# Kernel tuning notes

Measured on AMD Instinct MI355X. Metric: run time of the kernel, lower is better.

## Reference

```python
import jax, jax.numpy as jnp
import numpy as np

EPS = 1e-6
CONV_P = 3.0
GM_P = 2.0
NUM_NODES = 50000
NUM_EDGES = 600000
NUM_GRAPHS = 512
IN_DIM = 128
HID = 128
OUT_DIM = 64


def _scatter_mean(vals, index, num_segments):
    # scatter_mean with empty segments -> 0 (count clamped to 1)
    s = jax.ops.segment_sum(vals, index, num_segments=num_segments)
    cnt = jax.ops.segment_sum(jnp.ones((vals.shape[0],), vals.dtype), index,
                              num_segments=num_segments)
    return s / jnp.maximum(cnt, 1.0)[:, None]


def _signed_pow(v, p):
    return jnp.sign(v) * (jnp.abs(v) + EPS) ** p


def _spm_conv(x, W, b, src, dst, p):
    h = x @ W.T + b                      # [N, hid] linear
    msg = h[src]                          # gather x_j  [E, hid]
    t = _signed_pow(msg, p)
    pooled = _scatter_mean(t, dst, NUM_NODES)
    return _signed_pow(pooled, 1.0 / p)


def setup_inputs() -> dict:
    key = jax.random.key(0)
    ks = jax.random.split(key, 8)
    x = jax.random.normal(ks[0], (NUM_NODES, IN_DIM), jnp.float32)
    edge_index = jax.random.randint(ks[1], (2, NUM_EDGES), 0, NUM_NODES)
    batch = jnp.sort(jax.random.randint(ks[2], (NUM_NODES,), 0, NUM_GRAPHS))
    s1 = 1.0 / np.sqrt(IN_DIM)
    s2 = 1.0 / np.sqrt(HID)
    W1 = jax.random.uniform(ks[3], (HID, IN_DIM), jnp.float32, -s1, s1)
    b1 = jax.random.uniform(ks[4], (HID,), jnp.float32, -s1, s1)
    W2 = jax.random.uniform(ks[5], (HID, HID), jnp.float32, -s2, s2)
    b2 = jax.random.uniform(ks[6], (HID,), jnp.float32, -s2, s2)
    # final layer: orthogonal-init frozen weight (out_dim=64, hid=128)
    A = jax.random.normal(ks[7], (HID, OUT_DIM), jnp.float32)
    Q, _ = jnp.linalg.qr(A)
    Wout = Q.T                            # [OUT_DIM, HID], orthonormal rows
    bout = jax.random.uniform(jax.random.fold_in(key, 9), (OUT_DIM,),
                              jnp.float32, -s2, s2)
    return {"x": x, "W1": W1, "b1": b1, "W2": W2, "b2": b2,
            "Wout": Wout, "bout": bout, "edge_index": edge_index,
            "batch": batch}


def reference(x, W1, b1, W2, b2, Wout, bout, edge_index, batch):
    src, dst = edge_index[0], edge_index[1]
    h = _spm_conv(x, W1, b1, src, dst, CONV_P)
    h = jax.nn.relu(h)                    # relu between conv layers only
    h = _spm_conv(h, W2, b2, src, dst, CONV_P)
    # global generalized mean pool (signed)
    t = _signed_pow(h, GM_P)
    pooled = _scatter_mean(t, batch, NUM_GRAPHS)
    graph_repr = _signed_pow(pooled, 1.0 / GM_P)   # [G, HID]
    return graph_repr @ Wout.T + bout              # [G, OUT_DIM]
```

## Files before the change

kernel.cpp:

```cpp
#include <hip/hip_runtime.h>
#include <hip/hip_bf16.h>
#include <math.h>

#define N_NODES 50000
#define N_EDGES 600000
#define N_GRAPHS 512
#define DIM 128
#define OUTD 64
#define EPSV 1e-6f
#define BSTRIDE 64
#define EBLK 2344
#define PREP_BLK 64

typedef __attribute__((ext_vector_type(8))) short bf16x8;
typedef __attribute__((ext_vector_type(4))) float f32x4;

__device__ __forceinline__ float sgn(float v) {
    return (v > 0.f) ? 1.f : ((v < 0.f) ? -1.f : 0.f);
}

__device__ __forceinline__ float cube_signed(float v) {
    float m = fabsf(v) + EPSV;
    return sgn(v) * m * m * m;
}

__device__ __forceinline__ float cbrt_pos(float m) {
    return exp2f(log2f(m) * (1.0f / 3.0f));
}

__device__ __forceinline__ unsigned short f2bf(float f) {
    unsigned u = __float_as_uint(f);
    unsigned r = (u + 0x7fff + ((u >> 16) & 1)) >> 16;
    return (unsigned short)r;
}

__device__ __forceinline__ float bf2f(unsigned short h) {
    return __uint_as_float(((unsigned)h) << 16);
}

__device__ __forceinline__ void gather_acc8(const unsigned* __restrict__ T32,
                                            const int* __restrict__ bucket,
                                            int cnt, int lane, float acc[8]) {
    #pragma unroll
    for (int j = 0; j < 8; j++) acc[j] = 0.f;
    if (cnt <= 0) return;
    int myidx = bucket[lane];
    int sub = lane & 15, grp = lane >> 4;
    for (int i = 0; i < cnt; i += 16) {
        uint4 u[4];
        #pragma unroll
        for (int c = 0; c < 4; c++) {
            int eid = i + c * 4 + grp;
            int eidc = eid < cnt - 1 ? eid : cnt - 1;
            int s = __shfl(myidx, eidc, 64);
            u[c] = *(const uint4*)(T32 + (size_t)s * 64 + sub * 4);
        }
        #pragma unroll
        for (int c = 0; c < 4; c++) {
            int eid = i + c * 4 + grp;
            bool ok = eid < cnt;
            unsigned w0 = ok ? u[c].x : 0u;
            unsigned w1 = ok ? u[c].y : 0u;
            unsigned w2 = ok ? u[c].z : 0u;
            unsigned w3 = ok ? u[c].w : 0u;
            acc[0] += __uint_as_float(w0 << 16);
            acc[1] += __uint_as_float(w0 & 0xffff0000u);
            acc[2] += __uint_as_float(w1 << 16);
            acc[3] += __uint_as_float(w1 & 0xffff0000u);
            acc[4] += __uint_as_float(w2 << 16);
            acc[5] += __uint_as_float(w2 & 0xffff0000u);
            acc[6] += __uint_as_float(w3 << 16);
            acc[7] += __uint_as_float(w3 & 0xffff0000u);
        }
    }
    #pragma unroll
    for (int j = 0; j < 8; j++) {
        acc[j] += __shfl_xor(acc[j], 16, 64);
        acc[j] += __shfl_xor(acc[j], 32, 64);
    }
}


__global__ void build(const int* __restrict__ src, const int* __restrict__ dst,
                      int* __restrict__ deg, int* __restrict__ csr,
                      const float* __restrict__ W1, const float* __restrict__ W2,
                      unsigned short* __restrict__ W1hi, unsigned short* __restrict__ W1lo,
                      unsigned short* __restrict__ W2hi, unsigned short* __restrict__ W2lo,
                      const int* __restrict__ batch, int* __restrict__ gstart) {
    int b = blockIdx.x;
    if (b < EBLK) {
        int e = b * 256 + threadIdx.x;
        if (e < N_EDGES) {
            int d = dst[e];
            int slot = atomicAdd(&deg[d], 1);
            if (slot < BSTRIDE) csr[d * BSTRIDE + slot] = src[e];
        }
    } else {
        int i = (b - EBLK) * 256 + threadIdx.x;
        if (i < DIM * DIM) {
            float w = W1[i];
            unsigned short h = f2bf(w);
            W1hi[i] = h;
            W1lo[i] = f2bf(w - bf2f(h));
            w = W2[i];
            h = f2bf(w);
            W2hi[i] = h;
            W2lo[i] = f2bf(w - bf2f(h));
        }
        if (i <= N_GRAPHS) {
            int lo = 0, hi = N_NODES;
            while (lo < hi) {
                int mid = (lo + hi) >> 1;
                if (batch[mid] < i) lo = mid + 1; else hi = mid;
            }
            gstart[i] = lo;
        }
    }
}


__global__ __launch_bounds__(256) void linear_cube_mfma(const float* __restrict__ X,
                                                        const unsigned short* __restrict__ Whi,
                                                        const unsigned short* __restrict__ Wlo,
                                                        const float* __restrict__ B,
                                                        unsigned short* __restrict__ T) {
    int wave = threadIdx.x >> 6;
    int lane = threadIdx.x & 63;
    int tile = blockIdx.x * 4 + wave;
    if (tile >= N_NODES / 16) return;
    int n0 = tile * 16;
    int r = lane & 15;
    int g = lane >> 4;

    bf16x8 xh[4], xl[4];
    const float* xrow = X + (size_t)(n0 + r) * DIM + g * 8;
    #pragma unroll
    for (int kb = 0; kb < 4; kb++) {
        float4 a = *(const float4*)(xrow + kb * 32);
        float4 b = *(const float4*)(xrow + kb * 32 + 4);
        float v[8] = {a.x, a.y, a.z, a.w, b.x, b.y, b.z, b.w};
        #pragma unroll
        for (int j = 0; j < 8; j++) {
            unsigned short h = f2bf(v[j]);
            float rem = v[j] - bf2f(h);
            xh[kb][j] = (short)h;
            xl[kb][j] = (short)f2bf(rem);
        }
    }

    #pragma unroll
    for (int ct = 0; ct < 8; ct++) {
        const unsigned short* whbase = Whi + (size_t)(ct * 16 + r) * DIM + g * 8;
        const unsigned short* wlbase = Wlo + (size_t)(ct * 16 + r) * DIM + g * 8;
        f32x4 acc = {0.f, 0.f, 0.f, 0.f};
        #pragma unroll
        for (int kb = 0; kb < 4; kb++) {
            bf16x8 wh = *(const bf16x8*)(whbase + kb * 32);
            bf16x8 wl = *(const bf16x8*)(wlbase + kb * 32);
            acc = __builtin_amdgcn_mfma_f32_16x16x32_bf16(xh[kb], wh, acc, 0, 0, 0);
            acc = __builtin_amdgcn_mfma_f32_16x16x32_bf16(xl[kb], wh, acc, 0, 0, 0);
            acc = __builtin_amdgcn_mfma_f32_16x16x32_bf16(xh[kb], wl, acc, 0, 0, 0);
        }
        float bias = B[ct * 16 + r];
        #pragma unroll
        for (int q = 0; q < 4; q++) {
            int node = g * 4 + q;
            float h = acc[q] + bias;
            T[(size_t)(n0 + node) * DIM + ct * 16 + r] = f2bf(cube_signed(h));
        }
    }
}


__global__ __launch_bounds__(512) void agg_linear_cube(const unsigned* __restrict__ T32,
                                                       const int* __restrict__ deg,
                                                       const int* __restrict__ csr,
                                                       const unsigned short* __restrict__ Whi,
                                                       const unsigned short* __restrict__ Wlo,
                                                       const float* __restrict__ B,
                                                       unsigned short* __restrict__ Tout) {
    __shared__ float Pl[16][132];
    int wave = threadIdx.x >> 6;
    int lane = threadIdx.x & 63;
    int n0 = blockIdx.x * 16;
    int sub = lane & 15, grp = lane >> 4;

    #pragma unroll
    for (int q = 0; q < 2; q++) {
        int row = wave * 2 + q;
        int nd = n0 + row;
        int d = deg[nd];
        int cnt = d < BSTRIDE ? d : BSTRIDE;
        float acc[8];
        gather_acc8(T32, csr + (size_t)nd * BSTRIDE, cnt, lane, acc);
        float c = (float)(d > 1 ? d : 1);
        float m0 = acc[2 * grp] / c, m1 = acc[2 * grp + 1] / c;
        float r0 = fmaxf(sgn(m0) * cbrt_pos(fabsf(m0) + EPSV), 0.f);
        float r1 = fmaxf(sgn(m1) * cbrt_pos(fabsf(m1) + EPSV), 0.f);
        *(float2*)&Pl[row][sub * 8 + grp * 2] = make_float2(r0, r1);
    }
    __syncthreads();

    int r = lane & 15;
    int g = lane >> 4;
    bf16x8 xh[4], xl[4];
    #pragma unroll
    for (int kb = 0; kb < 4; kb++) {
        float4 va = *(const float4*)&Pl[r][kb * 32 + g * 8];
        float4 vb = *(const float4*)&Pl[r][kb * 32 + g * 8 + 4];
        float v[8] = {va.x, va.y, va.z, va.w, vb.x, vb.y, vb.z, vb.w};
        #pragma unroll
        for (int j = 0; j < 8; j++) {
            unsigned short h = f2bf(v[j]);
            xh[kb][j] = (short)h;
            xl[kb][j] = (short)f2bf(v[j] - bf2f(h));
        }
    }
    int ct = wave;
    const unsigned short* whbase = Whi + (size_t)(ct * 16 + r) * DIM + g * 8;
    const unsigned short* wlbase = Wlo + (size_t)(ct * 16 + r) * DIM + g * 8;
    f32x4 acc = {0.f, 0.f, 0.f, 0.f};
    #pragma unroll
    for (int kb = 0; kb < 4; kb++) {
        bf16x8 wh = *(const bf16x8*)(whbase + kb * 32);
        bf16x8 wl = *(const bf16x8*)(wlbase + kb * 32);
        acc = __builtin_amdgcn_mfma_f32_16x16x32_bf16(xh[kb], wh, acc, 0, 0, 0);
        acc = __builtin_amdgcn_mfma_f32_16x16x32_bf16(xl[kb], wh, acc, 0, 0, 0);
        acc = __builtin_amdgcn_mfma_f32_16x16x32_bf16(xh[kb], wl, acc, 0, 0, 0);
    }
    float bias = B[ct * 16 + r];
    #pragma unroll
    for (int q = 0; q < 4; q++) {
        int node = g * 4 + q;
        float h = acc[q] + bias;
        Tout[(size_t)(n0 + node) * DIM + ct * 16 + r] = f2bf(cube_signed(h));
    }
}


__global__ __launch_bounds__(256) void aggregate(const unsigned* __restrict__ T32,
                                                 const int* __restrict__ deg,
                                                 const int* __restrict__ csr,
                                                 float* __restrict__ P) {
    int nd = blockIdx.x * 4 + (threadIdx.x >> 6);
    if (nd >= N_NODES) return;
    int lane = threadIdx.x & 63;
    int sub = lane & 15, grp = lane >> 4;
    int d = deg[nd];
    int cnt = d < BSTRIDE ? d : BSTRIDE;
    float acc[8];
    gather_acc8(T32, csr + (size_t)nd * BSTRIDE, cnt, lane, acc);
    float c = (float)(d > 1 ? d : 1);
    float m0 = acc[2 * grp] / c, m1 = acc[2 * grp + 1] / c;
    float r0 = sgn(m0) * cbrt_pos(fabsf(m0) + EPSV);
    float r1 = sgn(m1) * cbrt_pos(fabsf(m1) + EPSV);
    *(float2*)(P + (size_t)nd * DIM + sub * 8 + grp * 2) = make_float2(r0, r1);
}


__global__ __launch_bounds__(128) void pool_final(const float* __restrict__ P,
                                                  const int* __restrict__ gstart,
                                                  const float* __restrict__ Wout,
                                                  const float* __restrict__ bout,
                                                  float* __restrict__ out) {
    __shared__ float R[DIM];
    __shared__ float partial[128];
    int g = blockIdx.x, f = threadIdx.x;
    int s = gstart[g], e = gstart[g + 1];
    float acc = 0.f;
    for (int i = s; i < e; i++) {
        float v = P[(size_t)i * DIM + f];
        float m = fabsf(v) + EPSV;
        acc += sgn(v) * m * m;
    }
    int cnt = e - s;
    float c = (float)(cnt > 1 ? cnt : 1);
    float mean = acc / c;
    R[f] = sgn(mean) * sqrtf(fabsf(mean) + EPSV);
    __syncthreads();

    int o = f & 63;
    int half = f >> 6;
    const float4* W4 = (const float4*)Wout + o * 32 + half * 16;
    const float4* R4 = (const float4*)R + half * 16;
    float a = 0.f;
    #pragma unroll
    for (int k = 0; k < 16; k++) {
        float4 w = W4[k];
        float4 r = R4[k];
        a += r.x * w.x + r.y * w.y + r.z * w.z + r.w * w.w;
    }
    partial[f] = a;
    __syncthreads();
    if (f < OUTD) out[(size_t)g * OUTD + f] = bout[f] + partial[f] + partial[f + 64];
}


extern "C" void kernel_launch(void* const* d_in, const int* in_sizes, int n_in,
                              void* d_out, int out_size, void* d_ws, size_t ws_size,
                              hipStream_t stream) {
    const float* x    = (const float*)d_in[0];
    const float* W1   = (const float*)d_in[1];
    const float* b1   = (const float*)d_in[2];
    const float* W2   = (const float*)d_in[3];
    const float* b2   = (const float*)d_in[4];
    const float* Wout = (const float*)d_in[5];
    const float* bout = (const float*)d_in[6];
    const int* edge   = (const int*)d_in[7];
    const int* batch  = (const int*)d_in[8];
    const int* srcp = edge;
    const int* dstp = edge + N_EDGES;
    float* out = (float*)d_out;

    char* ws = (char*)d_ws;
    size_t off = 0;
    auto alloc = [&](size_t bytes) -> char* {
        char* p = ws + off;
        off += (bytes + 255) / 256 * 256;
        return p;
    };
    unsigned short* T1 = (unsigned short*)alloc((size_t)N_NODES * DIM * 2);
    unsigned short* T2 = (unsigned short*)alloc((size_t)N_NODES * DIM * 2);
    float* P        = (float*)alloc((size_t)N_NODES * DIM * 4);
    int*   deg      = (int*)alloc((size_t)N_NODES * 4);
    int*   csr      = (int*)alloc((size_t)N_NODES * BSTRIDE * 4);
    int*   gstart   = (int*)alloc((size_t)(N_GRAPHS + 1) * 4);
    unsigned short* W1hi = (unsigned short*)alloc((size_t)DIM * DIM * 2);
    unsigned short* W1lo = (unsigned short*)alloc((size_t)DIM * DIM * 2);
    unsigned short* W2hi = (unsigned short*)alloc((size_t)DIM * DIM * 2);
    unsigned short* W2lo = (unsigned short*)alloc((size_t)DIM * DIM * 2);

    hipMemsetAsync(deg, 0, (size_t)N_NODES * 4, stream);
    build<<<EBLK + PREP_BLK, 256, 0, stream>>>(srcp, dstp, deg, csr,
                                               W1, W2, W1hi, W1lo, W2hi, W2lo,
                                               batch, gstart);

    const int TILES = N_NODES / 16;
    const int LBLK = (TILES + 3) / 4;
    const int ABLK = (N_NODES + 3) / 4;
    linear_cube_mfma<<<LBLK, 256, 0, stream>>>(x, W1hi, W1lo, b1, T1);
    agg_linear_cube<<<TILES, 512, 0, stream>>>((const unsigned*)T1, deg, csr,
                                               W2hi, W2lo, b2, T2);
    aggregate<<<ABLK, 256, 0, stream>>>((const unsigned*)T2, deg, csr, P);
    pool_final<<<N_GRAPHS, 128, 0, stream>>>(P, gstart, Wout, bout, out);
}
```

Before: 190.6 us.

## Use zero sentinel row to drop per-edge masking in neighbor gather

```diff
diff --git a/kernel.cpp b/kernel.cpp
--- a/kernel.cpp
+++ b/kernel.cpp
@@ -40,43 +40,37 @@
 
 __device__ __forceinline__ void gather_acc8(const unsigned* __restrict__ T32,
                                             const int* __restrict__ bucket,
-                                            int cnt, int lane, float acc[8]) {
-    #pragma unroll
-    for (int j = 0; j < 8; j++) acc[j] = 0.f;
-    if (cnt <= 0) return;
+                                            int cnt16, int lane, float2 acc[4]) {
+    #pragma unroll
+    for (int j = 0; j < 4; j++) acc[j] = make_float2(0.f, 0.f);
+    if (cnt16 <= 0) return;
     int myidx = bucket[lane];
     int sub = lane & 15, grp = lane >> 4;
-    for (int i = 0; i < cnt; i += 16) {
+    for (int i = 0; i < cnt16; i += 16) {
         uint4 u[4];
         #pragma unroll
         for (int c = 0; c < 4; c++) {
-            int eid = i + c * 4 + grp;
-            int eidc = eid < cnt - 1 ? eid : cnt - 1;
-            int s = __shfl(myidx, eidc, 64);
+            int s = __shfl(myidx, i + c * 4 + grp, 64);
             u[c] = *(const uint4*)(T32 + (size_t)s * 64 + sub * 4);
         }
         #pragma unroll
         for (int c = 0; c < 4; c++) {
-            int eid = i + c * 4 + grp;
-            bool ok = eid < cnt;
-            unsigned w0 = ok ? u[c].x : 0u;
-            unsigned w1 = ok ? u[c].y : 0u;
-            unsigned w2 = ok ? u[c].z : 0u;
-            unsigned w3 = ok ? u[c].w : 0u;
-            acc[0] += __uint_as_float(w0 << 16);
-            acc[1] += __uint_as_float(w0 & 0xffff0000u);
-            acc[2] += __uint_as_float(w1 << 16);
-            acc[3] += __uint_as_float(w1 & 0xffff0000u);
-            acc[4] += __uint_as_float(w2 << 16);
-            acc[5] += __uint_as_float(w2 & 0xffff0000u);
-            acc[6] += __uint_as_float(w3 << 16);
-            acc[7] += __uint_as_float(w3 & 0xffff0000u);
-        }
-    }
-    #pragma unroll
-    for (int j = 0; j < 8; j++) {
-        acc[j] += __shfl_xor(acc[j], 16, 64);
-        acc[j] += __shfl_xor(acc[j], 32, 64);
+            acc[0].x += __uint_as_float(u[c].x << 16);
+            acc[0].y += __uint_as_float(u[c].x & 0xffff0000u);
+            acc[1].x += __uint_as_float(u[c].y << 16);
+            acc[1].y += __uint_as_float(u[c].y & 0xffff0000u);
+            acc[2].x += __uint_as_float(u[c].z << 16);
+            acc[2].y += __uint_as_float(u[c].z & 0xffff0000u);
+            acc[3].x += __uint_as_float(u[c].w << 16);
+            acc[3].y += __uint_as_float(u[c].w & 0xffff0000u);
+        }
+    }
+    #pragma unroll
+    for (int j = 0; j < 4; j++) {
+        acc[j].x += __shfl_xor(acc[j].x, 16, 64);
+        acc[j].y += __shfl_xor(acc[j].y, 16, 64);
+        acc[j].x += __shfl_xor(acc[j].x, 32, 64);
+        acc[j].y += __shfl_xor(acc[j].y, 32, 64);
     }
 }
 
@@ -86,17 +80,19 @@
                       const float* __restrict__ W1, const float* __restrict__ W2,
                       unsigned short* __restrict__ W1hi, unsigned short* __restrict__ W1lo,
                       unsigned short* __restrict__ W2hi, unsigned short* __restrict__ W2lo,
-                      const int* __restrict__ batch, int* __restrict__ gstart) {
+                      const int* __restrict__ batch, int* __restrict__ gstart,
+                      unsigned* __restrict__ T1z, unsigned* __restrict__ T2z) {
     int b = blockIdx.x;
     if (b < EBLK) {
         int e = b * 256 + threadIdx.x;
         if (e < N_EDGES) {
             int d = dst[e];
             int slot = atomicAdd(&deg[d], 1);
-            if (slot < BSTRIDE) csr[d * BSTRIDE + slot] = src[e];
+            if (slot < BSTRIDE) csr[d * BSTRIDE + slot] = src[e] + 1;
         }
     } else {
         int i = (b - EBLK) * 256 + threadIdx.x;
+        if (i < 64) { T1z[i] = 0u; T2z[i] = 0u; }
         if (i < DIM * DIM) {
             float w = W1[i];
             unsigned short h = f2bf(w);
@@ -166,7 +162,7 @@
         for (int q = 0; q < 4; q++) {
             int node = g * 4 + q;
             float h = acc[q] + bias;
-            T[(size_t)(n0 + node) * DIM + ct * 16 + r] = f2bf(cube_signed(h));
+            T[(size_t)(n0 + node + 1) * DIM + ct * 16 + r] = f2bf(cube_signed(h));
         }
     }
 }
@@ -179,7 +175,8 @@
                                                        const unsigned short* __restrict__ Wlo,
                                                        const float* __restrict__ B,
                                                        unsigned short* __restrict__ Tout) {
-    __shared__ float Pl[16][132];
+    __shared__ __attribute__((aligned(16))) unsigned Phi[16][68];
+    __shared__ __attribute__((aligned(16))) unsigned Plo[16][68];
     int wave = threadIdx.x >> 6;
     int lane = threadIdx.x & 63;
     int n0 = blockIdx.x * 16;
@@ -191,13 +188,19 @@
         int nd = n0 + row;
         int d = deg[nd];
         int cnt = d < BSTRIDE ? d : BSTRIDE;
-        float acc[8];
-        gather_acc8(T32, csr + (size_t)nd * BSTRIDE, cnt, lane, acc);
+        int cnt16 = (cnt + 15) & ~15;
+        float2 acc[4];
+        gather_acc8(T32, csr + (size_t)nd * BSTRIDE, cnt16, lane, acc);
         float c = (float)(d > 1 ? d : 1);
-        float m0 = acc[2 * grp] / c, m1 = acc[2 * grp + 1] / c;
+        float m0 = acc[grp >> 1].x, m1 = acc[grp >> 1].y;
+        m0 = (grp == 0 ? acc[0].x : grp == 1 ? acc[1].x : grp == 2 ? acc[2].x : acc[3].x) / c;
+        m1 = (grp == 0 ? acc[0].y : grp == 1 ? acc[1].y : grp == 2 ? acc[2].y : acc[3].y) / c;
         float r0 = fmaxf(sgn(m0) * cbrt_pos(fabsf(m0) + EPSV), 0.f);
         float r1 = fmaxf(sgn(m1) * cbrt_pos(fabsf(m1) + EPSV), 0.f);
-        *(float2*)&Pl[row][sub * 8 + grp * 2] = make_float2(r0, r1);
+        unsigned short h0 = f2bf(r0), h1 = f2bf(r1);
+        unsigned short l0 = f2bf(r0 - bf2f(h0)), l1 = f2bf(r1 - bf2f(h1));
+        Phi[row][sub * 4 + grp] = (unsigned)h0 | ((unsigned)h1 << 16);
+        Plo[row][sub * 4 + grp] = (unsigned)l0 | ((unsigned)l1 << 16);
     }
     __syncthreads();
 
@@ -206,15 +209,8 @@
     bf16x8 xh[4], xl[4];
     #pragma unroll
     for (int kb = 0; kb < 4; kb++) {
-        float4 va = *(const float4*)&Pl[r][kb * 32 + g * 8];
-        float4 vb = *(const float4*)&Pl[r][kb * 32 + g * 8 + 4];
-        float v[8] = {va.x, va.y, va.z, va.w, vb.x, vb.y, vb.z, vb.w};
-        #pragma unroll
-        for (int j = 0; j < 8; j++) {
-            unsigned short h = f2bf(v[j]);
-            xh[kb][j] = (short)h;
-            xl[kb][j] = (short)f2bf(v[j] - bf2f(h));
-        }
+        xh[kb] = *(const bf16x8*)&Phi[r][kb * 16 + g * 4];
+        xl[kb] = *(const bf16x8*)&Plo[r][kb * 16 + g * 4];
     }
     int ct = wave;
     const unsigned short* whbase = Whi + (size_t)(ct * 16 + r) * DIM + g * 8;
@@ -233,7 +229,7 @@
     for (int q = 0; q < 4; q++) {
         int node = g * 4 + q;
         float h = acc[q] + bias;
-        Tout[(size_t)(n0 + node) * DIM + ct * 16 + r] = f2bf(cube_signed(h));
+        Tout[(size_t)(n0 + node + 1) * DIM + ct * 16 + r] = f2bf(cube_signed(h));
     }
 }
 
@@ -248,10 +244,12 @@
     int sub = lane & 15, grp = lane >> 4;
     int d = deg[nd];
     int cnt = d < BSTRIDE ? d : BSTRIDE;
-    float acc[8];
-    gather_acc8(T32, csr + (size_t)nd * BSTRIDE, cnt, lane, acc);
+    int cnt16 = (cnt + 15) & ~15;
+    float2 acc[4];
+    gather_acc8(T32, csr + (size_t)nd * BSTRIDE, cnt16, lane, acc);
     float c = (float)(d > 1 ? d : 1);
-    float m0 = acc[2 * grp] / c, m1 = acc[2 * grp + 1] / c;
+    float m0 = (grp == 0 ? acc[0].x : grp == 1 ? acc[1].x : grp == 2 ? acc[2].x : acc[3].x) / c;
+    float m1 = (grp == 0 ? acc[0].y : grp == 1 ? acc[1].y : grp == 2 ? acc[2].y : acc[3].y) / c;
     float r0 = sgn(m0) * cbrt_pos(fabsf(m0) + EPSV);
     float r1 = sgn(m1) * cbrt_pos(fabsf(m1) + EPSV);
     *(float2*)(P + (size_t)nd * DIM + sub * 8 + grp * 2) = make_float2(r0, r1);
@@ -319,8 +317,8 @@
         off += (bytes + 255) / 256 * 256;
         return p;
     };
-    unsigned short* T1 = (unsigned short*)alloc((size_t)N_NODES * DIM * 2);
-    unsigned short* T2 = (unsigned short*)alloc((size_t)N_NODES * DIM * 2);
+    unsigned short* T1 = (unsigned short*)alloc((size_t)(N_NODES + 1) * DIM * 2);
+    unsigned short* T2 = (unsigned short*)alloc((size_t)(N_NODES + 1) * DIM * 2);
     float* P        = (float*)alloc((size_t)N_NODES * DIM * 4);
     int*   deg      = (int*)alloc((size_t)N_NODES * 4);
     int*   csr      = (int*)alloc((size_t)N_NODES * BSTRIDE * 4);
@@ -331,9 +329,11 @@
     unsigned short* W2lo = (unsigned short*)alloc((size_t)DIM * DIM * 2);
 
     hipMemsetAsync(deg, 0, (size_t)N_NODES * 4, stream);
+    hipMemsetAsync(csr, 0, (size_t)N_NODES * BSTRIDE * 4, stream);
     build<<<EBLK + PREP_BLK, 256, 0, stream>>>(srcp, dstp, deg, csr,
                                                W1, W2, W1hi, W1lo, W2hi, W2lo,
-                                               batch, gstart);
+                                               batch, gstart,
+                                               (unsigned*)T1, (unsigned*)T2);
 
     const int TILES = N_NODES / 16;
     const int LBLK = (TILES + 3) / 4;
```

Measured after the change: 187.4 us. About the same (-1.7%).
